# Performance work log

Hardware: AMD Instinct MI355X
Metric: run time of the kernel (lower is better)

The kernel has to match this reference:

```python
import jax, jax.numpy as jnp
import numpy as np

N = 50000      # total nodes (batched graphs)
E = 800000     # edges per hop-set
B = 128        # number of graphs in batch
F_IN = 1024    # num_features_pro
D = 128        # hidden*16, heads=1


def setup_inputs() -> dict:
    key = jax.random.key(0)
    ks = jax.random.split(key, 32)
    s = 0.05
    def ei(k):
        return jax.random.randint(k, (2, E), 0, N, dtype=jnp.int32)
    inp = {
        'pro1_x': jax.random.normal(ks[0], (N, F_IN), jnp.float32),
        'pro1_ei1': ei(ks[1]), 'pro1_ei2': ei(ks[2]), 'pro1_ei3': ei(ks[3]),
        'pro1_batch': jnp.sort(jax.random.randint(ks[4], (N,), 0, B, dtype=jnp.int32)),
        'pro2_x': jax.random.normal(ks[5], (N, F_IN), jnp.float32),
        'pro2_ei1': ei(ks[6]), 'pro2_ei2': ei(ks[7]), 'pro2_ei3': ei(ks[8]),
        'pro2_batch': jnp.sort(jax.random.randint(ks[9], (N,), 0, B, dtype=jnp.int32)),
        # GATConv params (pro1_conv1 / pro2_conv1), shared across hop sets per branch
        'W1': jax.random.normal(ks[10], (F_IN, D), jnp.float32) * s,
        'a1_src': jax.random.normal(ks[11], (D,), jnp.float32) * s,
        'a1_dst': jax.random.normal(ks[12], (D,), jnp.float32) * s,
        'b1': jnp.zeros((D,), jnp.float32),
        'p1fc_W': jax.random.normal(ks[13], (D, D), jnp.float32) * s,
        'p1fc_b': jnp.zeros((D,), jnp.float32),
        'W2': jax.random.normal(ks[14], (F_IN, D), jnp.float32) * s,
        'a2_src': jax.random.normal(ks[15], (D,), jnp.float32) * s,
        'a2_dst': jax.random.normal(ks[16], (D,), jnp.float32) * s,
        'b2': jnp.zeros((D,), jnp.float32),
        'p2fc_W': jax.random.normal(ks[17], (D, D), jnp.float32) * s,
        'p2fc_b': jnp.zeros((D,), jnp.float32),
        'fc1_W': jax.random.normal(ks[18], (2 * D, 256), jnp.float32) * s,
        'fc1_b': jnp.zeros((256,), jnp.float32),
        'fc2_W': jax.random.normal(ks[19], (256, 64), jnp.float32) * s,
        'fc2_b': jnp.zeros((64,), jnp.float32),
        'out_W': jax.random.normal(ks[20], (64, 1), jnp.float32) * s,
        'out_b': jnp.zeros((1,), jnp.float32),
    }
    return inp


def _gat(x, ei, W, a_src, a_dst, b):
    # PyG GATConv, heads=1, add_self_loops=True, dropout off (eval)
    n = x.shape[0]
    h = x @ W                                   # [N, D]
    loops = jnp.arange(n, dtype=ei.dtype)
    src = jnp.concatenate([ei[0], loops])
    dst = jnp.concatenate([ei[1], loops])
    al_s = h @ a_src                            # [N]
    al_d = h @ a_dst
    e = jax.nn.leaky_relu(al_s[src] + al_d[dst], 0.2)   # per-edge logits
    m = jax.ops.segment_max(e, dst, num_segments=n)
    ex = jnp.exp(e - m[dst])
    denom = jax.ops.segment_sum(ex, dst, num_segments=n)
    alpha = ex / denom[dst]
    out = jax.ops.segment_sum(alpha[:, None] * h[src], dst, num_segments=n)
    return out + b


def _lrelu(v):
    return jax.nn.leaky_relu(v, 0.01)  # nn.LeakyReLU default slope


def _branch(x, e1, e2, e3, batch, W, a_s, a_d, b, fcW, fcb):
    h = _lrelu(_gat(x, e1, W, a_s, a_d, b))
    h = h + _lrelu(_gat(x, e2, W, a_s, a_d, b))
    h = h + _lrelu(_gat(x, e3, W, a_s, a_d, b))  # num_hops>=2 branch taken
    counts = jax.ops.segment_sum(jnp.ones((x.shape[0],), x.dtype), batch, num_segments=B)
    pooled = jax.ops.segment_sum(h, batch, num_segments=B) / jnp.maximum(counts, 1.0)[:, None]
    return _lrelu(pooled @ fcW + fcb)


def reference(pro1_x, pro1_ei1, pro1_ei2, pro1_ei3, pro1_batch,
              pro2_x, pro2_ei1, pro2_ei2, pro2_ei3, pro2_batch,
              W1, a1_src, a1_dst, b1, p1fc_W, p1fc_b,
              W2, a2_src, a2_dst, b2, p2fc_W, p2fc_b,
              fc1_W, fc1_b, fc2_W, fc2_b, out_W, out_b):
    x1 = _branch(pro1_x, pro1_ei1, pro1_ei2, pro1_ei3, pro1_batch, W1, a1_src, a1_dst, b1, p1fc_W, p1fc_b)
    x2 = _branch(pro2_x, pro2_ei1, pro2_ei2, pro2_ei3, pro2_batch, W2, a2_src, a2_dst, b2, p2fc_W, p2fc_b)
    xc = jnp.concatenate([x1, x2], axis=1)      # [B, 256]
    xc = _lrelu(xc @ fc1_W + fc1_b)
    xc = _lrelu(xc @ fc2_W + fc2_b)
    return jax.nn.sigmoid(xc @ out_W + out_b)   # [B, 1]
```

## Files before the change

kernel.cpp:

```cpp
#include <hip/hip_runtime.h>
#include <hip/hip_bf16.h>
#include <math.h>

#define N_NODES 50000
#define N_EDGES 800000
#define N_GRAPH 128
#define F_IN    1024
#define D_HID   128
#define NT3     (3*N_NODES)
#define LOG2E   1.44269504f

#define NPB_SH  9
#define NPB     512
#define NB      ((NT3 + NPB - 1) / NPB)
#define CAP     10240
#define EPB     4096
#define NBIN_PB ((3*N_EDGES + EPB - 1) / EPB)

typedef __bf16 bf16x8 __attribute__((ext_vector_type(8)));
typedef float  f32x4  __attribute__((ext_vector_type(4)));
typedef float  f32x2  __attribute__((ext_vector_type(2)));

__device__ __forceinline__ float lrelu01(float x){ return x > 0.f ? x : 0.01f*x; }
__device__ __forceinline__ float lrelu02(float x){ return x > 0.f ? x : 0.2f*x; }
__device__ __forceinline__ ushort f2bf(float v){
    __hip_bfloat16 hb = __float2bfloat16(v);
    return *reinterpret_cast<ushort*>(&hb);
}
__device__ __forceinline__ unsigned char f2fp8(float v){
    return (unsigned char)(__builtin_amdgcn_cvt_pk_fp8_f32(v, v, 0, false) & 0xFF);
}
__device__ __forceinline__ void fma8f8(uint2 u, float w, float* acc){
    f32x2 a = __builtin_amdgcn_cvt_pk_f32_fp8(u.x, false);
    f32x2 b = __builtin_amdgcn_cvt_pk_f32_fp8(u.x, true);
    f32x2 c = __builtin_amdgcn_cvt_pk_f32_fp8(u.y, false);
    f32x2 d = __builtin_amdgcn_cvt_pk_f32_fp8(u.y, true);
    acc[0] += w*a[0]; acc[1] += w*a[1]; acc[2] += w*b[0]; acc[3] += w*b[1];
    acc[4] += w*c[0]; acc[5] += w*c[1]; acc[6] += w*d[0]; acc[7] += w*d[1];
}

__global__ void k_prep(const float* __restrict__ W0, const float* __restrict__ W1,
                       ushort* __restrict__ Wt, int* __restrict__ gcur){
    int b = blockIdx.x, t = threadIdx.x;
    if (b < 1024){
        int idx = b*256 + t;
        int br  = idx >> 17;
        int r   = idx & 131071;
        int n = r >> 10, k = r & 1023;
        const float* W = br ? W1 : W0;
        Wt[idx] = f2bf(W[k*D_HID + n]);
    } else {
        for (int i=t; i<2*NB; i+=256) gcur[i] = 0;
    }
}

#define BM  32
#define BK  64
#define LDP 72

__global__ __launch_bounds__(256) void k_gemm(const float* __restrict__ X0, const float* __restrict__ X1,
                                              const ushort* __restrict__ Wt,
                                              const float* __restrict__ as0, const float* __restrict__ ad0,
                                              const float* __restrict__ as1, const float* __restrict__ ad1,
                                              unsigned char* __restrict__ H8,
                                              float* __restrict__ als, float* __restrict__ ald){
    __shared__ ushort As[BM*LDP];
    __shared__ ushort Bs[D_HID*LDP];
    __shared__ float alp[4][2][BM];
    int br = blockIdx.y;
    const float*  X   = br ? X1 : X0;
    const float*  asr = br ? as1 : as0;
    const float*  adr = br ? ad1 : ad0;
    const ushort* Wtb = Wt + (size_t)br*D_HID*F_IN;
    unsigned char* Hbb = H8 + (size_t)br*N_NODES*D_HID;

    int tid  = threadIdx.x;
    int m0   = blockIdx.x * BM;
    int lane = tid & 63;
    int wave = tid >> 6;
    int l15 = lane & 15, l4 = lane >> 4;
    int wcol = wave * 32;

    float4 pa[2];
    uint4  pb[4];

    auto loadA = [&](int kt){
        #pragma unroll
        for (int i=0;i<2;i++){
            int q = tid + i*256; int row = q >> 4; int kq = (q & 15) << 2;
            int gr = m0 + row;
            pa[i] = (gr < N_NODES) ? *reinterpret_cast<const float4*>(X + (size_t)gr*F_IN + kt + kq)
                                   : make_float4(0.f,0.f,0.f,0.f);
        }
    };
    auto loadB = [&](int kt){
        #pragma unroll
        for (int i=0;i<4;i++){
            int q = tid + i*256; int row = q >> 3; int ck = q & 7;
            pb[i] = *reinterpret_cast<const uint4*>(Wtb + row*F_IN + kt + ck*8);
        }
    };
    auto stage = [&](){
        #pragma unroll
        for (int i=0;i<2;i++){
            int q = tid + i*256; int row = q >> 4; int kq = (q & 15) << 2;
            ushort4 b; b.x=f2bf(pa[i].x); b.y=f2bf(pa[i].y); b.z=f2bf(pa[i].z); b.w=f2bf(pa[i].w);
            *reinterpret_cast<ushort4*>(&As[row*LDP + kq]) = b;
        }
        #pragma unroll
        for (int i=0;i<4;i++){
            int q = tid + i*256; int row = q >> 3; int ck = q & 7;
            *reinterpret_cast<uint2*>(&Bs[row*LDP + ck*8])     = make_uint2(pb[i].x, pb[i].y);
            *reinterpret_cast<uint2*>(&Bs[row*LDP + ck*8 + 4]) = make_uint2(pb[i].z, pb[i].w);
        }
    };

    f32x4 acc[2][2];
    #pragma unroll
    for (int i=0;i<2;i++) for (int j=0;j<2;j++) acc[i][j] = (f32x4){0.f,0.f,0.f,0.f};

    loadA(0); loadB(0);
    for (int kt = 0; kt < F_IN; kt += BK) {
        stage();
        __syncthreads();
        if (kt + BK < F_IN){ loadA(kt+BK); loadB(kt+BK); }
        #pragma unroll
        for (int kk = 0; kk < BK; kk += 32) {
            bf16x8 af[2], bfr[2];
            #pragma unroll
            for (int mi=0;mi<2;mi++)
                af[mi] = *reinterpret_cast<const bf16x8*>(&As[(mi*16+l15)*LDP + kk + l4*8]);
            #pragma unroll
            for (int ni=0;ni<2;ni++)
                bfr[ni] = *reinterpret_cast<const bf16x8*>(&Bs[(wcol+ni*16+l15)*LDP + kk + l4*8]);
            #pragma unroll
            for (int mi=0;mi<2;mi++)
                #pragma unroll
                for (int ni=0;ni<2;ni++)
                    acc[mi][ni] = __builtin_amdgcn_mfma_f32_16x16x32_bf16(af[mi], bfr[ni], acc[mi][ni], 0,0,0);
        }
        __syncthreads();
    }

    float asv[2], adv[2];
    #pragma unroll
    for (int ni=0;ni<2;ni++){
        int c = wcol + ni*16 + l15;
        asv[ni] = asr[c]; adv[ni] = adr[c];
    }
    #pragma unroll
    for (int mi=0;mi<2;mi++){
        #pragma unroll
        for (int jj=0;jj<4;jj++){
            int rrel = mi*16 + l4*4 + jj;
            int r = m0 + rrel;
            float ps = 0.f, pd = 0.f;
            #pragma unroll
            for (int ni=0;ni<2;ni++){
                float v = acc[mi][ni][jj];
                ps += v*asv[ni]; pd += v*adv[ni];
                if (r < N_NODES){
                    int c = wcol + ni*16 + l15;
                    Hbb[(size_t)r*D_HID + c] = f2fp8(v);
                }
            }
            #pragma unroll
            for (int o=1;o<16;o<<=1){ ps += __shfl_xor(ps,o); pd += __shfl_xor(pd,o); }
            if (l15 == 0){ alp[wave][0][rrel] = ps; alp[wave][1][rrel] = pd; }
        }
    }
    __syncthreads();
    if (tid < BM){
        int r = m0 + tid;
        if (r < N_NODES){
            float s_ = alp[0][0][tid]+alp[1][0][tid]+alp[2][0][tid]+alp[3][0][tid];
            float d_ = alp[0][1][tid]+alp[1][1][tid]+alp[2][1][tid]+alp[3][1][tid];
            als[br*N_NODES + r] = s_;
            ald[br*N_NODES + r] = d_;
        }
    }
}

__global__ __launch_bounds__(256) void k_bin(const int* __restrict__ e10, const int* __restrict__ e20,
                                             const int* __restrict__ e30,
                                             const int* __restrict__ e11, const int* __restrict__ e21,
                                             const int* __restrict__ e31,
                                             int* __restrict__ gcur, uint* __restrict__ pairs){
    __shared__ int hist[NB];
    __shared__ int start[NB];
    int blk = blockIdx.x;
    int br    = blk / NBIN_PB;
    int chunk = blk - br*NBIN_PB;
    int tid = threadIdx.x;
    for (int b=tid; b<NB; b+=256) hist[b]=0;
    __syncthreads();
    long base = (long)chunk * EPB;
    int  myb[16]; uint mypk[16];
    #pragma unroll
    for (int i=0;i<16;i++){
        long idx = base + i*256 + tid;
        int b = -1; uint pk = 0;
        if (idx < 3L*N_EDGES){
            int hop = (idx >= 2L*N_EDGES) ? 2 : (idx >= (long)N_EDGES) ? 1 : 0;
            int e   = (int)(idx - (long)hop*N_EDGES);
            const int* ei = (br==0) ? ((hop==0)?e10:(hop==1)?e20:e30)
                                    : ((hop==0)?e11:(hop==1)?e21:e31);
            int src = ei[e];
            int vd  = hop*N_NODES + ei[N_EDGES + e];
            b   = vd >> NPB_SH;
            pk  = (uint)src | ((uint)(vd & (NPB-1)) << 16);
            atomicAdd(&hist[b], 1);
        }
        myb[i]=b; mypk[i]=pk;
    }
    __syncthreads();
    for (int b=tid; b<NB; b+=256){
        int h = hist[b];
        start[b] = (h>0) ? atomicAdd(&gcur[br*NB + b], h) : 0;
    }
    __syncthreads();
    for (int b=tid; b<NB; b+=256) hist[b] = start[b];
    __syncthreads();
    #pragma unroll
    for (int i=0;i<16;i++){
        int b = myb[i];
        if (b >= 0){
            int pos = atomicAdd(&hist[b], 1);
            if (pos < CAP) pairs[((size_t)(br*NB + b))*CAP + pos] = mypk[i];
        }
    }
}

__global__ __launch_bounds__(256) void k_localcsr(const int* __restrict__ gcur,
                                                  const uint* __restrict__ pairs,
                                                  int* __restrict__ offs3, int* __restrict__ esrc){
    __shared__ int sc[512];
    __shared__ int deg[NPB];
    __shared__ int cur[NPB];
    __shared__ int ss[256];
    int gb = blockIdx.x;
    int br = gb / NB, bb = gb - br*NB;
    int t = threadIdx.x;
    sc[t]     = (t < NB)       ? min(gcur[br*NB + t], CAP) : 0;
    sc[t+256] = (t+256 < NB)   ? min(gcur[br*NB + t+256], CAP) : 0;
    __syncthreads();
    for (int o=1;o<512;o<<=1){
        int v0 = (t>=o)     ? sc[t-o]     : 0;
        int v1 = (t+256>=o) ? sc[t+256-o] : 0;
        __syncthreads();
        sc[t] += v0; sc[t+256] += v1;
        __syncthreads();
    }
    int base = (bb==0) ? 0 : sc[bb-1];
    int cnt  = sc[bb] - base;
    int* offsb = offs3 + (size_t)br*(NT3+1);
    if (bb == NB-1 && t == 0) offsb[NT3] = sc[NB-1];

    deg[t]=0; deg[t+256]=0;
    __syncthreads();
    const uint* pbuf = pairs + ((size_t)(br*NB + bb))*CAP;
    for (int i=t; i<cnt; i+=256) atomicAdd(&deg[pbuf[i] >> 16], 1);
    __syncthreads();
    int a0 = deg[2*t], a1 = deg[2*t+1];
    int ps = a0 + a1;
    ss[t] = ps; __syncthreads();
    for (int o=1;o<256;o<<=1){
        int u = (t>=o) ? ss[t-o] : 0;
        __syncthreads(); ss[t] += u; __syncthreads();
    }
    int ex = ss[t] - ps;
    __syncthreads();
    deg[2*t] = ex; deg[2*t+1] = ex + a0;
    cur[2*t] = ex; cur[2*t+1] = ex + a0;
    __syncthreads();
    int vd0 = bb << NPB_SH;
    for (int l=t; l<NPB; l+=256){
        int vd = vd0 + l;
        if (vd < NT3) offsb[vd] = base + deg[l];
    }
    int* esrcb = esrc + (size_t)br*3*N_EDGES;
    for (int i=t; i<cnt; i+=256){
        uint p = pbuf[i];
        int pos = atomicAdd(&cur[p >> 16], 1);
        esrcb[base + pos] = (int)(p & 0xFFFFu);
    }
}

__global__ __launch_bounds__(256) void k_gat3(const int* __restrict__ offs3, const int* __restrict__ esrc3,
                     const float* __restrict__ als, const float* __restrict__ ald,
                     const uint2* __restrict__ H8,
                     const float* __restrict__ bv0, const float* __restrict__ bv1,
                     float* __restrict__ hacc){
    __shared__ uint2 sh[4][64];
    int br = blockIdx.y;
    const int*   offs = offs3 + (size_t)br*(NT3+1);
    const int*   esrc = esrc3 + (size_t)br*3*N_EDGES;
    const float* alsb = als + br*N_NODES;
    const float* aldb = ald + br*N_NODES;
    const uint2* H8b  = H8 + (size_t)br*N_NODES*16;
    const float* bvec = br ? bv1 : bv0;
    float*       hb   = hacc + (size_t)br*N_NODES*D_HID;

    int lane = threadIdx.x & 63;
    int wl   = threadIdx.x >> 6;
    int d = blockIdx.x*4 + wl;
    if (d >= N_NODES) return;
    int g  = lane >> 4;
    int fl = lane & 15;
    float aldd  = aldb[d];
    float eself = lrelu02(alsb[d] + aldd);
    float exs   = __builtin_amdgcn_exp2f(eself * LOG2E);
    uint2 hs = H8b[(size_t)d*16 + fl];
    float hself[8];
    { f32x2 a = __builtin_amdgcn_cvt_pk_f32_fp8(hs.x, false);
      f32x2 b = __builtin_amdgcn_cvt_pk_f32_fp8(hs.x, true);
      f32x2 c = __builtin_amdgcn_cvt_pk_f32_fp8(hs.y, false);
      f32x2 d2 = __builtin_amdgcn_cvt_pk_f32_fp8(hs.y, true);
      hself[0]=a[0];hself[1]=a[1];hself[2]=b[0];hself[3]=b[1];
      hself[4]=c[0];hself[5]=c[1];hself[6]=d2[0];hself[7]=d2[1]; }
    float bvv[8];
    #pragma unroll
    for (int k=0;k<8;k++) bvv[k] = bvec[fl*8+k];
    float tot[8] = {0.f,0.f,0.f,0.f,0.f,0.f,0.f,0.f};

    for (int hop=0; hop<3; hop++){
        int s0 = offs[hop*N_NODES + d];
        int s1 = offs[hop*N_NODES + d + 1];
        int deg = s1 - s0;
        float acc[8];
        #pragma unroll
        for (int k=0;k<8;k++) acc[k] = (g==0) ? exs*hself[k] : 0.f;
        float es = 0.f;
        for (int base=0; base<deg; base+=64){
            int j = base + lane;
            int s = 0; float ex = 0.f;
            if (j < deg){
                s = esrc[s0 + j];
                ex = __builtin_amdgcn_exp2f(lrelu02(alsb[s] + aldd) * LOG2E);
            }
            es += ex;
            sh[wl][lane] = make_uint2((uint)s, __float_as_uint(ex));
            int cnt = min(64, deg - base);
            int i = g;
            for (; i + 4 < cnt; i += 8){
                uint2 seA = sh[wl][i];
                uint2 seB = sh[wl][i+4];
                uint2 hvA = H8b[(size_t)seA.x*16 + fl];
                uint2 hvB = H8b[(size_t)seB.x*16 + fl];
                fma8f8(hvA, __uint_as_float(seA.y), acc);
                fma8f8(hvB, __uint_as_float(seB.y), acc);
            }
            if (i < cnt){
                uint2 se = sh[wl][i];
                uint2 hv = H8b[(size_t)se.x*16 + fl];
                fma8f8(hv, __uint_as_float(se.y), acc);
            }
        }
        for (int o=32;o;o>>=1) es += __shfl_xor(es,o);
        #pragma unroll
        for (int k=0;k<8;k++){
            acc[k] += __shfl_xor(acc[k], 16);
            acc[k] += __shfl_xor(acc[k], 32);
        }
        float inv = 1.f / (es + exs);
        #pragma unroll
        for (int k=0;k<8;k++) tot[k] += lrelu01(acc[k]*inv + bvv[k]);
    }
    if (g == 0){
        float4 w0 = make_float4(tot[0],tot[1],tot[2],tot[3]);
        float4 w1 = make_float4(tot[4],tot[5],tot[6],tot[7]);
        *reinterpret_cast<float4*>(hb + (size_t)d*D_HID + fl*8)     = w0;
        *reinterpret_cast<float4*>(hb + (size_t)d*D_HID + fl*8 + 4) = w1;
    }
}

__global__ __launch_bounds__(256) void k_pool_fc(const float* __restrict__ hacc,
                    const int* __restrict__ b0, const int* __restrict__ b1,
                    const float* __restrict__ pW0, const float* __restrict__ pb0,
                    const float* __restrict__ pW1, const float* __restrict__ pb1,
                    float* __restrict__ xb){
    __shared__ float sums[2][128];
    __shared__ float pl[128];
    int br = blockIdx.y;
    const float* hb   = hacc + (size_t)br*N_NODES*D_HID;
    const int*   batch= br ? b1 : b0;
    const float* fcW  = br ? pW1 : pW0;
    const float* fcb  = br ? pb1 : pb0;
    int g = blockIdx.x;
    int t = threadIdx.x;
    int lo=0, hi=N_NODES;
    while (lo<hi){ int mid=(lo+hi)>>1; if (batch[mid] < g) lo=mid+1; else hi=mid; }
    int s = lo;
    lo = s; hi = N_NODES;
    while (lo<hi){ int mid=(lo+hi)>>1; if (batch[mid] < g+1) lo=mid+1; else hi=mid; }
    int e = lo;
    int f = t & 127, half = t >> 7;
    float sum = 0.f;
    for (int n=s+half; n<e; n+=2) sum += hb[(size_t)n*D_HID + f];
    sums[half][f] = sum;
    __syncthreads();
    if (t < 128){
        float cnt = (float)(e - s);
        pl[t] = (sums[0][t] + sums[1][t]) / fmaxf(cnt, 1.0f);
    }
    __syncthreads();
    if (t < 128){
        float a = fcb[t];
        for (int k=0;k<128;k++) a += pl[k]*fcW[k*128 + t];
        xb[(br*N_GRAPH + g)*128 + t] = lrelu01(a);
    }
}

__global__ __launch_bounds__(256) void k_final(const float* __restrict__ xb,
                      const float* __restrict__ fc1W, const float* __restrict__ fc1b,
                      const float* __restrict__ fc2W, const float* __restrict__ fc2b,
                      const float* __restrict__ outW, const float* __restrict__ outb,
                      float* __restrict__ out){
    __shared__ float xc[256], y1[256], y2[64];
    int g = blockIdx.x, t = threadIdx.x;
    xc[t] = (t < 128) ? xb[g*128 + t] : xb[(N_GRAPH + g)*128 + (t-128)];
    __syncthreads();
    float a = fc1b[t];
    for (int k=0;k<256;k++) a += xc[k]*fc1W[k*256 + t];
    y1[t] = lrelu01(a);
    __syncthreads();
    if (t < 64){
        float a2 = fc2b[t];
        for (int k=0;k<256;k++) a2 += y1[k]*fc2W[k*64 + t];
        y2[t] = lrelu01(a2);
    }
    __syncthreads();
    if (t == 0){
        float z = outb[0];
        for (int k=0;k<64;k++) z += y2[k]*outW[k];
        out[g] = 1.f/(1.f + expf(-z));
    }
}

extern "C" void kernel_launch(void* const* d_in, const int* in_sizes, int n_in,
                              void* d_out, int out_size, void* d_ws, size_t ws_size,
                              hipStream_t stream){
    const float* X0 = (const float*)d_in[0];
    const float* X1 = (const float*)d_in[5];
    const int *e10=(const int*)d_in[1], *e20=(const int*)d_in[2], *e30=(const int*)d_in[3];
    const int *e11=(const int*)d_in[6], *e21=(const int*)d_in[7], *e31=(const int*)d_in[8];
    const int *b0=(const int*)d_in[4], *b1=(const int*)d_in[9];
    const float *W0=(const float*)d_in[10], *W1=(const float*)d_in[16];
    const float *as0=(const float*)d_in[11], *ad0=(const float*)d_in[12];
    const float *as1=(const float*)d_in[17], *ad1=(const float*)d_in[18];
    const float *bv0=(const float*)d_in[13], *bv1=(const float*)d_in[19];
    const float *pW0=(const float*)d_in[14], *pb0=(const float*)d_in[15];
    const float *pW1=(const float*)d_in[20], *pb1=(const float*)d_in[21];
    const float *fc1W=(const float*)d_in[22], *fc1b=(const float*)d_in[23];
    const float *fc2W=(const float*)d_in[24], *fc2b=(const float*)d_in[25];
    const float *outW=(const float*)d_in[26], *outb=(const float*)d_in[27];
    float* out = (float*)d_out;

    char* ws = (char*)d_ws;
    size_t o = 0;
    auto alloc = [&](size_t bytes)->char*{ char* p = ws + o; o += (bytes + 511) & ~(size_t)511; return p; };
    unsigned char* H8 = (unsigned char*)alloc((size_t)2*N_NODES*D_HID);
    float*  hacc  = (float*) alloc((size_t)2*N_NODES*D_HID*4);
    float*  als   = (float*) alloc((size_t)2*N_NODES*4);
    float*  ald   = (float*) alloc((size_t)2*N_NODES*4);
    int*    offs3 = (int*)   alloc((size_t)2*(NT3+1)*4);
    int*    esrc3 = (int*)   alloc((size_t)2*3*N_EDGES*4);
    int*    gcur  = (int*)   alloc((size_t)2*NB*4);
    uint*   pairs = (uint*)  alloc((size_t)2*NB*CAP*4);
    ushort* Wt    = (ushort*)alloc((size_t)2*D_HID*F_IN*2);
    float*  xb    = (float*) alloc((size_t)2*N_GRAPH*D_HID*4);

    k_prep    <<<1025, 256, 0, stream>>>(W0, W1, Wt, gcur);
    k_gemm    <<<dim3((N_NODES+BM-1)/BM, 2), 256, 0, stream>>>(X0, X1, Wt, as0, ad0, as1, ad1, H8, als, ald);
    k_bin     <<<2*NBIN_PB, 256, 0, stream>>>(e10, e20, e30, e11, e21, e31, gcur, pairs);
    k_localcsr<<<2*NB, 256, 0, stream>>>(gcur, pairs, offs3, esrc3);
    k_gat3    <<<dim3((N_NODES+3)/4, 2), 256, 0, stream>>>(offs3, esrc3, als, ald, (const uint2*)H8, bv0, bv1, hacc);
    k_pool_fc <<<dim3(N_GRAPH, 2), 256, 0, stream>>>(hacc, b0, b1, pW0, pb0, pW1, pb1, xb);
    k_final   <<<N_GRAPH, 256, 0, stream>>>(xb, fc1W, fc1b, fc2W, fc2b, outW, outb, out);
}
```

Before: 433.6 us.

## Load GEMM fragments directly from global memory into registers, skipping LDS

```diff
diff --git a/kernel.cpp b/kernel.cpp
--- a/kernel.cpp
+++ b/kernel.cpp
@@ -20,6 +20,7 @@
 typedef __bf16 bf16x8 __attribute__((ext_vector_type(8)));
 typedef float  f32x4  __attribute__((ext_vector_type(4)));
 typedef float  f32x2  __attribute__((ext_vector_type(2)));
+typedef ushort u16x8  __attribute__((ext_vector_type(8)));
 
 __device__ __forceinline__ float lrelu01(float x){ return x > 0.f ? x : 0.01f*x; }
 __device__ __forceinline__ float lrelu02(float x){ return x > 0.f ? x : 0.2f*x; }
@@ -29,6 +30,12 @@
 }
 __device__ __forceinline__ unsigned char f2fp8(float v){
     return (unsigned char)(__builtin_amdgcn_cvt_pk_fp8_f32(v, v, 0, false) & 0xFF);
+}
+__device__ __forceinline__ bf16x8 cvt8(float4 a, float4 b){
+    u16x8 u;
+    u[0]=f2bf(a.x); u[1]=f2bf(a.y); u[2]=f2bf(a.z); u[3]=f2bf(a.w);
+    u[4]=f2bf(b.x); u[5]=f2bf(b.y); u[6]=f2bf(b.z); u[7]=f2bf(b.w);
+    return *reinterpret_cast<bf16x8*>(&u);
 }
 __device__ __forceinline__ void fma8f8(uint2 u, float w, float* acc){
     f32x2 a = __builtin_amdgcn_cvt_pk_f32_fp8(u.x, false);
@@ -54,9 +61,7 @@
     }
 }
 
-#define BM  32
-#define BK  64
-#define LDP 72
+#define BM  64
 
 __global__ __launch_bounds__(256) void k_gemm(const float* __restrict__ X0, const float* __restrict__ X1,
                                               const ushort* __restrict__ Wt,
@@ -64,9 +69,7 @@
                                               const float* __restrict__ as1, const float* __restrict__ ad1,
                                               unsigned char* __restrict__ H8,
                                               float* __restrict__ als, float* __restrict__ ald){
-    __shared__ ushort As[BM*LDP];
-    __shared__ ushort Bs[D_HID*LDP];
-    __shared__ float alp[4][2][BM];
+    __shared__ float alp[2][2][2][32];
     int br = blockIdx.y;
     const float*  X   = br ? X1 : X0;
     const float*  asr = br ? as1 : as0;
@@ -78,105 +81,98 @@
     int m0   = blockIdx.x * BM;
     int lane = tid & 63;
     int wave = tid >> 6;
+    int wr = wave >> 1, wc = wave & 1;
     int l15 = lane & 15, l4 = lane >> 4;
-    int wcol = wave * 32;
-
-    float4 pa[2];
-    uint4  pb[4];
+
+    int r0 = min(m0 + wr*32 + l15,      N_NODES-1);
+    int r1 = min(m0 + wr*32 + 16 + l15, N_NODES-1);
+    const float* Xp0 = X + (size_t)r0*F_IN + l4*8;
+    const float* Xp1 = X + (size_t)r1*F_IN + l4*8;
+    const ushort* Wp = Wtb + (size_t)(wc*64 + l15)*F_IN + l4*8;
+
+    float4 pa[2][2][2];
+    uint4  pb[4][2];
 
     auto loadA = [&](int kt){
         #pragma unroll
-        for (int i=0;i<2;i++){
-            int q = tid + i*256; int row = q >> 4; int kq = (q & 15) << 2;
-            int gr = m0 + row;
-            pa[i] = (gr < N_NODES) ? *reinterpret_cast<const float4*>(X + (size_t)gr*F_IN + kt + kq)
-                                   : make_float4(0.f,0.f,0.f,0.f);
+        for (int kki=0;kki<2;kki++){
+            #pragma unroll
+            for (int h=0;h<2;h++){
+                pa[0][kki][h] = *reinterpret_cast<const float4*>(Xp0 + kt + kki*32 + h*4);
+                pa[1][kki][h] = *reinterpret_cast<const float4*>(Xp1 + kt + kki*32 + h*4);
+            }
         }
     };
     auto loadB = [&](int kt){
         #pragma unroll
-        for (int i=0;i<4;i++){
-            int q = tid + i*256; int row = q >> 3; int ck = q & 7;
-            pb[i] = *reinterpret_cast<const uint4*>(Wtb + row*F_IN + kt + ck*8);
+        for (int ni=0;ni<4;ni++){
+            #pragma unroll
+            for (int kki=0;kki<2;kki++)
+                pb[ni][kki] = *reinterpret_cast<const uint4*>(Wp + (size_t)ni*16*F_IN + kt + kki*32);
         }
     };
-    auto stage = [&](){
-        #pragma unroll
-        for (int i=0;i<2;i++){
-            int q = tid + i*256; int row = q >> 4; int kq = (q & 15) << 2;
-            ushort4 b; b.x=f2bf(pa[i].x); b.y=f2bf(pa[i].y); b.z=f2bf(pa[i].z); b.w=f2bf(pa[i].w);
-            *reinterpret_cast<ushort4*>(&As[row*LDP + kq]) = b;
-        }
-        #pragma unroll
-        for (int i=0;i<4;i++){
-            int q = tid + i*256; int row = q >> 3; int ck = q & 7;
-            *reinterpret_cast<uint2*>(&Bs[row*LDP + ck*8])     = make_uint2(pb[i].x, pb[i].y);
-            *reinterpret_cast<uint2*>(&Bs[row*LDP + ck*8 + 4]) = make_uint2(pb[i].z, pb[i].w);
-        }
-    };
-
-    f32x4 acc[2][2];
-    #pragma unroll
-    for (int i=0;i<2;i++) for (int j=0;j<2;j++) acc[i][j] = (f32x4){0.f,0.f,0.f,0.f};
+
+    f32x4 acc[2][4];
+    #pragma unroll
+    for (int i=0;i<2;i++) for (int j=0;j<4;j++) acc[i][j] = (f32x4){0.f,0.f,0.f,0.f};
 
     loadA(0); loadB(0);
-    for (int kt = 0; kt < F_IN; kt += BK) {
-        stage();
-        __syncthreads();
-        if (kt + BK < F_IN){ loadA(kt+BK); loadB(kt+BK); }
-        #pragma unroll
-        for (int kk = 0; kk < BK; kk += 32) {
-            bf16x8 af[2], bfr[2];
-            #pragma unroll
-            for (int mi=0;mi<2;mi++)
-                af[mi] = *reinterpret_cast<const bf16x8*>(&As[(mi*16+l15)*LDP + kk + l4*8]);
-            #pragma unroll
-            for (int ni=0;ni<2;ni++)
-                bfr[ni] = *reinterpret_cast<const bf16x8*>(&Bs[(wcol+ni*16+l15)*LDP + kk + l4*8]);
+    for (int kt = 0; kt < F_IN; kt += 64){
+        bf16x8 af[2][2], bfr[4][2];
+        #pragma unroll
+        for (int mi=0;mi<2;mi++)
+            #pragma unroll
+            for (int kki=0;kki<2;kki++)
+                af[mi][kki] = cvt8(pa[mi][kki][0], pa[mi][kki][1]);
+        #pragma unroll
+        for (int ni=0;ni<4;ni++)
+            #pragma unroll
+            for (int kki=0;kki<2;kki++)
+                bfr[ni][kki] = *reinterpret_cast<bf16x8*>(&pb[ni][kki]);
+        if (kt + 64 < F_IN){ loadA(kt+64); loadB(kt+64); }
+        #pragma unroll
+        for (int kki=0;kki<2;kki++)
             #pragma unroll
             for (int mi=0;mi<2;mi++)
                 #pragma unroll
-                for (int ni=0;ni<2;ni++)
-                    acc[mi][ni] = __builtin_amdgcn_mfma_f32_16x16x32_bf16(af[mi], bfr[ni], acc[mi][ni], 0,0,0);
-        }
-        __syncthreads();
-    }
-
-    float asv[2], adv[2];
-    #pragma unroll
-    for (int ni=0;ni<2;ni++){
-        int c = wcol + ni*16 + l15;
+                for (int ni=0;ni<4;ni++)
+                    acc[mi][ni] = __builtin_amdgcn_mfma_f32_16x16x32_bf16(af[mi][kki], bfr[ni][kki], acc[mi][ni], 0,0,0);
+    }
+
+    float asv[4], adv[4];
+    #pragma unroll
+    for (int ni=0;ni<4;ni++){
+        int c = wc*64 + ni*16 + l15;
         asv[ni] = asr[c]; adv[ni] = adr[c];
     }
     #pragma unroll
     for (int mi=0;mi<2;mi++){
         #pragma unroll
         for (int jj=0;jj<4;jj++){
-            int rrel = mi*16 + l4*4 + jj;
-            int r = m0 + rrel;
+            int rr32 = mi*16 + l4*4 + jj;
+            int r = m0 + wr*32 + rr32;
             float ps = 0.f, pd = 0.f;
             #pragma unroll
-            for (int ni=0;ni<2;ni++){
+            for (int ni=0;ni<4;ni++){
                 float v = acc[mi][ni][jj];
                 ps += v*asv[ni]; pd += v*adv[ni];
                 if (r < N_NODES){
-                    int c = wcol + ni*16 + l15;
+                    int c = wc*64 + ni*16 + l15;
                     Hbb[(size_t)r*D_HID + c] = f2fp8(v);
                 }
             }
             #pragma unroll
             for (int o=1;o<16;o<<=1){ ps += __shfl_xor(ps,o); pd += __shfl_xor(pd,o); }
-            if (l15 == 0){ alp[wave][0][rrel] = ps; alp[wave][1][rrel] = pd; }
-        }
-    }
-    __syncthreads();
-    if (tid < BM){
-        int r = m0 + tid;
+            if (l15 == 0){ alp[wr][wc][0][rr32] = ps; alp[wr][wc][1][rr32] = pd; }
+        }
+    }
+    __syncthreads();
+    if (tid < 64){
+        int wr2 = tid >> 5, rr = tid & 31;
+        int r = m0 + wr2*32 + rr;
         if (r < N_NODES){
-            float s_ = alp[0][0][tid]+alp[1][0][tid]+alp[2][0][tid]+alp[3][0][tid];
-            float d_ = alp[0][1][tid]+alp[1][1][tid]+alp[2][1][tid]+alp[3][1][tid];
-            als[br*N_NODES + r] = s_;
-            ald[br*N_NODES + r] = d_;
+            als[br*N_NODES + r] = alp[wr2][0][0][rr] + alp[wr2][1][0][rr];
+            ald[br*N_NODES + r] = alp[wr2][0][1][rr] + alp[wr2][1][1][rr];
         }
     }
 }
```

New measurement: 526.8 us. 1.21x slower.
